# Optimization experiments

Measured on AMD Instinct MI355X. Metric: run time of the kernel, lower is better.

## Reference

```python
import jax, jax.numpy as jnp
import numpy as np

KB = 0.0019872041      # Boltzmann constant, kcal/(mol*K)
TEMP = 300.0
ALPHA = 10.0
BW = 0.15              # Gaussian KDE bandwidth
PAIR_I = jnp.array([0, 0, 0, 1, 1, 2])
PAIR_J = jnp.array([1, 2, 3, 2, 3, 3])

B, N_ATOMS = 512, 1024
G, L, K, D = 256, 8, 128, 6


def setup_inputs() -> dict:
    key = jax.random.key(0)
    k1, k2, k3, k4, k5, k6 = jax.random.split(key, 6)
    positions = jax.random.normal(k1, (B, N_ATOMS, 3), dtype=jnp.float32) * 2.0
    # KDE training samples live in 6-dim distance space (positive, few Angstroms)
    kde_samples = jax.random.uniform(k2, (G, L, K, D), dtype=jnp.float32) * 5.0
    weight = jax.random.uniform(k3, (G, L), dtype=jnp.float32)
    offset = jax.random.normal(k4, (G, L), dtype=jnp.float32)
    atom_idxs = jax.random.randint(k5, (G, L, 4), 0, N_ATOMS)
    group_sizes = jax.random.randint(k6, (G,), 0, L)  # clamped to >=1 in reference
    return {"positions": positions, "kde_samples": kde_samples, "weight": weight,
            "offset": offset, "atom_idxs": atom_idxs, "group_sizes": group_sizes}


def reference(positions, kde_samples, weight, offset, atom_idxs, group_sizes):
    Gn, Ln, Kn, Dn = kde_samples.shape
    # Gather the 4 vertices of every loss: [B, G, L, 4, 3]
    vp = positions[:, atom_idxs]
    # 6 pairwise distances per loss: [B, G, L, 6]
    diff = vp[..., PAIR_I, :] - vp[..., PAIR_J, :]
    dists = jnp.sqrt(jnp.sum(diff * diff, axis=-1) + 1e-12)
    # Gaussian KDE log-density over the K training samples, expanded squared
    x2 = jnp.sum(dists * dists, axis=-1)          # [B,G,L]
    mu2 = jnp.sum(kde_samples * kde_samples, -1)  # [G,L,K]
    xmu = jnp.einsum('bgld,glkd->bglk', dists, kde_samples)
    sq = x2[..., None] + mu2[None] - 2.0 * xmu    # [B,G,L,K]
    log_norm = jnp.log(jnp.float32(Kn)) + 0.5 * Dn * jnp.log(2.0 * jnp.pi * BW * BW)
    logP = jax.nn.logsumexp(-sq / (2.0 * BW * BW), axis=-1) - log_norm  # [B,G,L]
    energy = -KB * TEMP * logP
    scaled = energy * weight + offset             # [B,G,L]
    # Ragged group reduction: min over the valid losses of each group
    sizes = jnp.maximum(group_sizes, 1)
    mask = jnp.arange(Ln)[None, :] < sizes[:, None]        # [G,L]
    group_min = jnp.min(jnp.where(mask, scaled, jnp.inf), axis=-1)  # [B,G]
    # soft-min across groups
    return -jax.nn.logsumexp(-ALPHA * group_min, axis=-1) / ALPHA   # [B]
```

## Files before the change

### kernel.cpp

```cpp
#include <hip/hip_runtime.h>

#define NB 512
#define NATOMS 1024
#define NG 256
#define NL 8
#define NK 128

#define KBT 0.59616123f
#define ALPHA_C 10.0f
#define LN2 0.6931471805599453f
#define LOG2E 1.4426950408889634f
#define INV2BW2 22.222221f
#define SCALE2 (INV2BW2 * LOG2E)
#define LOG_NORM (-1.0170649f)

#define WL_CAP 2048
#define FILL_BLOCKS 128

__device__ __forceinline__ float fexp2(float x) { return __builtin_amdgcn_exp2f(x); }
__device__ __forceinline__ float flog2(float x) { return __builtin_amdgcn_logf(x); }

__device__ __forceinline__ unsigned fkey(float f) {
  unsigned u = __float_as_uint(f);
  return (u & 0x80000000u) ? ~u : (u | 0x80000000u);
}
__device__ __forceinline__ float funkey(unsigned k) {
  unsigned u = (k & 0x80000000u) ? (k ^ 0x80000000u) : ~k;
  return __uint_as_float(u);
}

__device__ __forceinline__ float wred_min(float v) {
#pragma unroll
  for (int m = 32; m >= 1; m >>= 1) v = fminf(v, __shfl_xor(v, m, 64));
  return v;
}
__device__ __forceinline__ float wred_sum(float v) {
#pragma unroll
  for (int m = 32; m >= 1; m >>= 1) v += __shfl_xor(v, m, 64);
  return v;
}

__global__ __launch_bounds__(256) void build_worklist(
    const int* __restrict__ gsizes, int* __restrict__ wl,
    uint4* __restrict__ gmin_u4) {
  const int t = threadIdx.x;
  if (blockIdx.x != 0) {
    const unsigned F = 0xFFFFFFFFu;
    gmin_u4[(blockIdx.x - 1) * 256 + t] = make_uint4(F, F, F, F);
    return;
  }
  const int lane = t & 63, wid = t >> 6;
  int gs = gsizes[t];
  int nl = gs < 1 ? 1 : (gs > NL ? NL : gs);
  int x = nl;
#pragma unroll
  for (int m = 1; m < 64; m <<= 1) {
    int y = __shfl_up(x, m, 64);
    if (lane >= m) x += y;
  }
  __shared__ int wsum[4];
  if (lane == 63) wsum[wid] = x;
  __syncthreads();
  int off = 0;
  for (int i = 0; i < wid; ++i) off += wsum[i];
  int inc = off + x, exc = inc - nl;
  for (int j = 0; j < nl; ++j) wl[exc + j] = (t << 3) | j;
  if (t == 255) wl[WL_CAP] = inc;
}

__global__ __launch_bounds__(256) void stage1_kernel(
    const float* __restrict__ positions, const float* __restrict__ kde,
    const float* __restrict__ weight, const float* __restrict__ offs,
    const int* __restrict__ atom_idxs, const int* __restrict__ wl,
    unsigned* __restrict__ gmin_u) {
  const int w = blockIdx.x >> 1;
  const int bq = blockIdx.x & 1;
  const int count = wl[WL_CAP];
  if (w >= count) return;
  const int e = wl[w];
  const int g = e >> 3, l = e & 7;
  const int gl = g * NL + l;

  __shared__ __align__(16) float tab[NK][8];

  const int t = threadIdx.x;
  const float* kb = kde + (size_t)gl * NK * 6;
  if (t < NK) {
    const float* mp = kb + t * 6;
    float m0 = mp[0], m1 = mp[1], m2 = mp[2], m3 = mp[3], m4 = mp[4], m5 = mp[5];
    float mu2 = m0 * m0 + m1 * m1 + m2 * m2 + m3 * m3 + m4 * m4 + m5 * m5;
    const float cf = 2.0f * SCALE2;
    float4 lo = make_float4(m0 * cf, m1 * cf, m2 * cf, m3 * cf);
    float4 hi = make_float4(m4 * cf, m5 * cf, -mu2 * SCALE2, 0.0f);
    *reinterpret_cast<float4*>(&tab[t][0]) = lo;
    *reinterpret_cast<float4*>(&tab[t][4]) = hi;
  }
  __syncthreads();

  const int b = bq * 256 + t;
  const int4 idx = *reinterpret_cast<const int4*>(atom_idxs + (gl << 2));
  const int ids[4] = {idx.x, idx.y, idx.z, idx.w};
  const float* pb = positions + (size_t)b * NATOMS * 3;
  float ax[4], ay[4], az[4];
#pragma unroll
  for (int j = 0; j < 4; ++j) {
    const float* pp = pb + ids[j] * 3;
    ax[j] = pp[0]; ay[j] = pp[1]; az[j] = pp[2];
  }
  const int PI_[6] = {0, 0, 0, 1, 1, 2};
  const int PJ_[6] = {1, 2, 3, 2, 3, 3};
  float d[6]; float x2 = 0.0f;
#pragma unroll
  for (int q = 0; q < 6; ++q) {
    float dx = ax[PI_[q]] - ax[PJ_[q]];
    float dy = ay[PI_[q]] - ay[PJ_[q]];
    float dz = az[PI_[q]] - az[PJ_[q]];
    float dd = dx * dx + dy * dy + dz * dz + 1e-12f;
    d[q] = sqrtf(dd);
    x2 += d[q] * d[q];
  }
  const float c2 = -x2 * SCALE2;

  float m_[4] = {-1e30f, -1e30f, -1e30f, -1e30f};
  float s_[4] = {0.0f, 0.0f, 0.0f, 0.0f};
  for (int k0 = 0; k0 < NK; k0 += 16) {
#pragma unroll
    for (int j = 0; j < 4; ++j) {
      const int kk = k0 + (j << 2);
      float v[4];
#pragma unroll
      for (int i = 0; i < 4; ++i) {
        const float4* r = reinterpret_cast<const float4*>(&tab[kk + i][0]);
        float4 A = r[0], Bv = r[1];
        float vv = Bv.z;
        vv = fmaf(A.x, d[0], vv);
        vv = fmaf(A.y, d[1], vv);
        vv = fmaf(A.z, d[2], vv);
        vv = fmaf(A.w, d[3], vv);
        vv = fmaf(Bv.x, d[4], vv);
        vv = fmaf(Bv.y, d[5], vv);
        v[i] = vv;
      }
      float gm = fmaxf(fmaxf(v[0], v[1]), fmaxf(v[2], v[3]));
      float p = fexp2(v[0] - gm) + fexp2(v[1] - gm)
              + fexp2(v[2] - gm) + fexp2(v[3] - gm);
      float nm = fmaxf(m_[j], gm);
      s_[j] = fmaf(s_[j], fexp2(m_[j] - nm), p * fexp2(gm - nm));
      m_[j] = nm;
    }
  }
  float M = fmaxf(fmaxf(m_[0], m_[1]), fmaxf(m_[2], m_[3]));
  float S = s_[0] * fexp2(m_[0] - M) + s_[1] * fexp2(m_[1] - M)
          + s_[2] * fexp2(m_[2] - M) + s_[3] * fexp2(m_[3] - M);

  float lse2 = c2 + M + flog2(S);
  float logP = lse2 * LN2 - LOG_NORM;
  float scaled = -KBT * logP * weight[gl] + offs[gl];
  atomicMin(&gmin_u[g * NB + b], fkey(scaled));
}

__global__ __launch_bounds__(256) void stage2_kernel(
    const unsigned* __restrict__ gmin_u, float* __restrict__ out) {
  const int b = blockIdx.x;
  const int t = threadIdx.x;
  const int lane = t & 63;
  const int wid = t >> 6;
  float v = funkey(gmin_u[t * NB + b]);
  __shared__ float sm[4], ss[4];
  float m = wred_min(v);
  if (lane == 0) sm[wid] = m;
  __syncthreads();
  float M = fminf(fminf(sm[0], sm[1]), fminf(sm[2], sm[3]));
  float e = fexp2(-ALPHA_C * LOG2E * (v - M));
  float s = wred_sum(e);
  if (lane == 0) ss[wid] = s;
  __syncthreads();
  if (t == 0) {
    float S = ss[0] + ss[1] + ss[2] + ss[3];
    out[b] = M - flog2(S) * LN2 / ALPHA_C;
  }
}

extern "C" void kernel_launch(void* const* d_in, const int* in_sizes, int n_in,
                              void* d_out, int out_size, void* d_ws, size_t ws_size,
                              hipStream_t stream) {
  const float* positions = (const float*)d_in[0];
  const float* kde       = (const float*)d_in[1];
  const float* weight    = (const float*)d_in[2];
  const float* offs      = (const float*)d_in[3];
  const int*   atom_idxs = (const int*)d_in[4];
  const int*   gsizes    = (const int*)d_in[5];
  float* out = (float*)d_out;

  unsigned* gmin_u = (unsigned*)d_ws;
  int* wl = (int*)d_ws + (size_t)NG * NB;

  build_worklist<<<dim3(1 + FILL_BLOCKS), dim3(256), 0, stream>>>(
      gsizes, wl, (uint4*)gmin_u);
  stage1_kernel<<<dim3(NG * NL * 2), dim3(256), 0, stream>>>(
      positions, kde, weight, offs, atom_idxs, wl, gmin_u);
  stage2_kernel<<<dim3(NB), dim3(256), 0, stream>>>(gmin_u, out);
}
```

Before: 41.89 us.

## Register-block four batch elements per thread to reuse LDS KDE table reads

Each thread now computes four batch elements for one loss, loading each KDE table row from shared memory once and applying it to four distance vectors. Each block holds two worklist entries with separate tables, and the grid shrinks fourfold. This reduces shared-memory read traffic per FMA, in exchange for higher register pressure and fewer waves to hide latency.

```diff
diff --git a/kernel.cpp b/kernel.cpp
--- a/kernel.cpp
+++ b/kernel.cpp
@@ -73,72 +73,83 @@
     const float* __restrict__ weight, const float* __restrict__ offs,
     const int* __restrict__ atom_idxs, const int* __restrict__ wl,
     unsigned* __restrict__ gmin_u) {
-  const int w = blockIdx.x >> 1;
-  const int bq = blockIdx.x & 1;
+  const int bid = blockIdx.x;
   const int count = wl[WL_CAP];
-  if (w >= count) return;
-  const int e = wl[w];
-  const int g = e >> 3, l = e & 7;
-  const int gl = g * NL + l;
-
-  __shared__ __align__(16) float tab[NK][8];
+  if ((bid << 1) >= count) return;
 
   const int t = threadIdx.x;
-  const float* kb = kde + (size_t)gl * NK * 6;
-  if (t < NK) {
-    const float* mp = kb + t * 6;
+  const int ep = t >> 7;
+  const int li = t & 127;
+  const int w = (bid << 1) + ep;
+  const bool active = (w < count);
+
+  __shared__ __align__(16) float tab[2][NK][8];
+
+  int gl = 0;
+  if (active) {
+    const int e = wl[w];
+    gl = (e >> 3) * NL + (e & 7);
+    const float* mp = kde + (size_t)gl * NK * 6 + (size_t)li * 6;
     float m0 = mp[0], m1 = mp[1], m2 = mp[2], m3 = mp[3], m4 = mp[4], m5 = mp[5];
     float mu2 = m0 * m0 + m1 * m1 + m2 * m2 + m3 * m3 + m4 * m4 + m5 * m5;
     const float cf = 2.0f * SCALE2;
-    float4 lo = make_float4(m0 * cf, m1 * cf, m2 * cf, m3 * cf);
-    float4 hi = make_float4(m4 * cf, m5 * cf, -mu2 * SCALE2, 0.0f);
-    *reinterpret_cast<float4*>(&tab[t][0]) = lo;
-    *reinterpret_cast<float4*>(&tab[t][4]) = hi;
-  }
-  __syncthreads();
-
-  const int b = bq * 256 + t;
+    *reinterpret_cast<float4*>(&tab[ep][li][0]) =
+        make_float4(m0 * cf, m1 * cf, m2 * cf, m3 * cf);
+    *reinterpret_cast<float4*>(&tab[ep][li][4]) =
+        make_float4(m4 * cf, m5 * cf, -mu2 * SCALE2, 0.0f);
+  }
+  __syncthreads();
+  if (!active) return;
+
   const int4 idx = *reinterpret_cast<const int4*>(atom_idxs + (gl << 2));
   const int ids[4] = {idx.x, idx.y, idx.z, idx.w};
-  const float* pb = positions + (size_t)b * NATOMS * 3;
-  float ax[4], ay[4], az[4];
-#pragma unroll
-  for (int j = 0; j < 4; ++j) {
-    const float* pp = pb + ids[j] * 3;
-    ax[j] = pp[0]; ay[j] = pp[1]; az[j] = pp[2];
-  }
   const int PI_[6] = {0, 0, 0, 1, 1, 2};
   const int PJ_[6] = {1, 2, 3, 2, 3, 3};
-  float d[6]; float x2 = 0.0f;
-#pragma unroll
-  for (int q = 0; q < 6; ++q) {
-    float dx = ax[PI_[q]] - ax[PJ_[q]];
-    float dy = ay[PI_[q]] - ay[PJ_[q]];
-    float dz = az[PI_[q]] - az[PJ_[q]];
-    float dd = dx * dx + dy * dy + dz * dz + 1e-12f;
-    d[q] = sqrtf(dd);
-    x2 += d[q] * d[q];
-  }
-  const float c2 = -x2 * SCALE2;
+  float d[4][6], c2[4];
+#pragma unroll
+  for (int j = 0; j < 4; ++j) {
+    const int b = (j << 7) + li;
+    const float* pb = positions + (size_t)b * NATOMS * 3;
+    float ax[4], ay[4], az[4];
+#pragma unroll
+    for (int a = 0; a < 4; ++a) {
+      const float* pp = pb + ids[a] * 3;
+      ax[a] = pp[0]; ay[a] = pp[1]; az[a] = pp[2];
+    }
+    float x2 = 0.0f;
+#pragma unroll
+    for (int q = 0; q < 6; ++q) {
+      float dx = ax[PI_[q]] - ax[PJ_[q]];
+      float dy = ay[PI_[q]] - ay[PJ_[q]];
+      float dz = az[PI_[q]] - az[PJ_[q]];
+      float dd = dx * dx + dy * dy + dz * dz + 1e-12f;
+      d[j][q] = sqrtf(dd);
+      x2 += d[j][q] * d[j][q];
+    }
+    c2[j] = -x2 * SCALE2;
+  }
 
   float m_[4] = {-1e30f, -1e30f, -1e30f, -1e30f};
   float s_[4] = {0.0f, 0.0f, 0.0f, 0.0f};
-  for (int k0 = 0; k0 < NK; k0 += 16) {
+  for (int k0 = 0; k0 < NK; k0 += 4) {
+    float4 A[4], Bv[4];
+#pragma unroll
+    for (int i = 0; i < 4; ++i) {
+      const float4* r = reinterpret_cast<const float4*>(&tab[ep][k0 + i][0]);
+      A[i] = r[0]; Bv[i] = r[1];
+    }
 #pragma unroll
     for (int j = 0; j < 4; ++j) {
-      const int kk = k0 + (j << 2);
       float v[4];
 #pragma unroll
       for (int i = 0; i < 4; ++i) {
-        const float4* r = reinterpret_cast<const float4*>(&tab[kk + i][0]);
-        float4 A = r[0], Bv = r[1];
-        float vv = Bv.z;
-        vv = fmaf(A.x, d[0], vv);
-        vv = fmaf(A.y, d[1], vv);
-        vv = fmaf(A.z, d[2], vv);
-        vv = fmaf(A.w, d[3], vv);
-        vv = fmaf(Bv.x, d[4], vv);
-        vv = fmaf(Bv.y, d[5], vv);
+        float vv = Bv[i].z;
+        vv = fmaf(A[i].x, d[j][0], vv);
+        vv = fmaf(A[i].y, d[j][1], vv);
+        vv = fmaf(A[i].z, d[j][2], vv);
+        vv = fmaf(A[i].w, d[j][3], vv);
+        vv = fmaf(Bv[i].x, d[j][4], vv);
+        vv = fmaf(Bv[i].y, d[j][5], vv);
         v[i] = vv;
       }
       float gm = fmaxf(fmaxf(v[0], v[1]), fmaxf(v[2], v[3]));
@@ -149,14 +160,16 @@
       m_[j] = nm;
     }
   }
-  float M = fmaxf(fmaxf(m_[0], m_[1]), fmaxf(m_[2], m_[3]));
-  float S = s_[0] * fexp2(m_[0] - M) + s_[1] * fexp2(m_[1] - M)
-          + s_[2] * fexp2(m_[2] - M) + s_[3] * fexp2(m_[3] - M);
-
-  float lse2 = c2 + M + flog2(S);
-  float logP = lse2 * LN2 - LOG_NORM;
-  float scaled = -KBT * logP * weight[gl] + offs[gl];
-  atomicMin(&gmin_u[g * NB + b], fkey(scaled));
+
+  const float wgt = weight[gl], off = offs[gl];
+  const int g = gl >> 3;
+#pragma unroll
+  for (int j = 0; j < 4; ++j) {
+    float lse2 = c2[j] + m_[j] + flog2(s_[j]);
+    float logP = lse2 * LN2 - LOG_NORM;
+    float scaled = -KBT * logP * wgt + off;
+    atomicMin(&gmin_u[g * NB + (j << 7) + li], fkey(scaled));
+  }
 }
 
 __global__ __launch_bounds__(256) void stage2_kernel(
@@ -197,7 +210,7 @@
 
   build_worklist<<<dim3(1 + FILL_BLOCKS), dim3(256), 0, stream>>>(
       gsizes, wl, (uint4*)gmin_u);
-  stage1_kernel<<<dim3(NG * NL * 2), dim3(256), 0, stream>>>(
+  stage1_kernel<<<dim3(WL_CAP / 2), dim3(256), 0, stream>>>(
       positions, kde, weight, offs, atom_idxs, wl, gmin_u);
   stage2_kernel<<<dim3(NB), dim3(256), 0, stream>>>(gmin_u, out);
 }
```

New measurement: 48.65 us. +16.1%, slower.
